# Kernel tuning notes

Hardware: AMD Instinct MI355X
Metric: run time of the kernel (lower is better)

Reference implementation:

```python
import jax, jax.numpy as jnp
import numpy as np

N_NODES = 50000
N_EDGES = 800000
NUM_GRAPHS = 128
FEAT = 128
HID = 64
NUM_LAYERS = 3
OUT = 2
K = 30
LATENT = HID * NUM_LAYERS + 1  # 193 = conv1 kernel size & stride


def _lin(k, i, o):
    s = 1.0 / np.sqrt(i)
    return jax.random.uniform(k, (i, o), jnp.float32, -s, s)


def setup_inputs() -> dict:
    key = jax.random.key(0)
    ks = jax.random.split(key, 16)
    x = jax.random.normal(ks[0], (N_NODES, FEAT), jnp.float32)
    edge_index = jax.random.randint(ks[1], (2, N_EDGES), 0, N_NODES, dtype=jnp.int64)
    batch = jnp.sort(jax.random.randint(ks[2], (N_NODES,), 0, NUM_GRAPHS, dtype=jnp.int64))
    w0 = _lin(ks[3], FEAT, HID); b0 = jnp.zeros((HID,), jnp.float32)
    w1 = _lin(ks[4], HID, HID);  b1 = jnp.zeros((HID,), jnp.float32)
    w2 = _lin(ks[5], HID, HID);  b2 = jnp.zeros((HID,), jnp.float32)
    w3 = _lin(ks[6], HID, 1);    b3 = jnp.zeros((1,), jnp.float32)
    conv1_w = jax.random.normal(ks[7], (16, 1, LATENT), jnp.float32) * (1.0 / np.sqrt(LATENT))
    conv1_b = jnp.zeros((16,), jnp.float32)
    conv2_w = jax.random.normal(ks[8], (32, 16, 5), jnp.float32) * (1.0 / np.sqrt(16 * 5))
    conv2_b = jnp.zeros((32,), jnp.float32)
    dense_dim = (int((K - 2) / 2 + 1) - 5 + 1) * 32  # 352
    lin1_w = _lin(ks[9], dense_dim, 256); lin1_b = jnp.zeros((256,), jnp.float32)
    lin2_w = _lin(ks[10], 256, OUT);      lin2_b = jnp.zeros((OUT,), jnp.float32)
    return dict(x=x, edge_index=edge_index, batch=batch,
                w0=w0, b0=b0, w1=w1, b1=b1, w2=w2, b2=b2, w3=w3, b3=b3,
                conv1_w=conv1_w, conv1_b=conv1_b, conv2_w=conv2_w, conv2_b=conv2_b,
                lin1_w=lin1_w, lin1_b=lin1_b, lin2_w=lin2_w, lin2_b=lin2_b)


def _gcn(h_in, w, b, src, dst, norm, n):
    # GCNConv: out_i = sum_j d_i^-1/2 d_j^-1/2 (x_j W) over A+I, plus bias
    h = h_in @ w
    msg = h[src] * norm[:, None]  # gather over edges (incl. self loops)
    return jax.ops.segment_sum(msg, dst, num_segments=n) + b


def _sort_pool(x, batch, k, g):
    # per-graph descending sort on last channel, top-k, zero-pad
    n, d = x.shape
    order = jnp.lexsort((-x[:, -1], batch))  # primary: batch asc, secondary: last feat desc
    xs, bs = x[order], batch[order]
    counts = jax.ops.segment_sum(jnp.ones((n,), jnp.int32), batch, num_segments=g)
    starts = jnp.cumsum(counts) - counts
    rank = jnp.arange(n) - starts[bs]
    slot = jnp.where(rank < k, rank, k)  # overflow nodes dumped in slot k (discarded)
    out = jnp.zeros((g, k + 1, d), x.dtype).at[bs, slot].set(xs)
    return out[:, :k].reshape(g, k * d)


def _conv1d(z, w, stride):
    return jax.lax.conv_general_dilated(z, w, window_strides=(stride,), padding='VALID',
                                        dimension_numbers=('NCH', 'OIH', 'NCH'))


def reference(x, edge_index, batch, w0, b0, w1, b1, w2, b2, w3, b3,
              conv1_w, conv1_b, conv2_w, conv2_b, lin1_w, lin1_b, lin2_w, lin2_b):
    n = x.shape[0]
    loop = jnp.arange(n, dtype=edge_index.dtype)
    src = jnp.concatenate([edge_index[0], loop])
    dst = jnp.concatenate([edge_index[1], loop])
    deg = jax.ops.segment_sum(jnp.ones_like(src, jnp.float32), dst, num_segments=n)
    dinv = jnp.where(deg > 0, jax.lax.rsqrt(deg), 0.0)
    norm = dinv[src] * dinv[dst]

    h1 = jnp.tanh(_gcn(x,  w0, b0, src, dst, norm, n))
    h2 = jnp.tanh(_gcn(h1, w1, b1, src, dst, norm, n))
    h3 = jnp.tanh(_gcn(h2, w2, b2, src, dst, norm, n))
    h4 = jnp.tanh(_gcn(h3, w3, b3, src, dst, norm, n))
    hcat = jnp.concatenate([h1, h2, h3, h4], axis=-1)  # [N, 193]

    p = _sort_pool(hcat, batch, K, NUM_GRAPHS)  # [G, K*193]
    z = p[:, None, :]                                   # [G, 1, K*193]
    z = jax.nn.relu(_conv1d(z, conv1_w, LATENT) + conv1_b[None, :, None])  # [G,16,K]
    g, c, l = z.shape
    z = z.reshape(g, c, l // 2, 2).max(axis=-1)         # MaxPool1d(2,2) -> [G,16,15]
    z = jax.nn.relu(_conv1d(z, conv2_w, 1) + conv2_b[None, :, None])       # [G,32,11]
    z = z.reshape(g, -1)                                # [G,352]
    z = jax.nn.relu(z @ lin1_w + lin1_b)
    # dropout is identity in eval mode
    return z @ lin2_w + lin2_b
```

## Files before the change

kernel.cpp:

```cpp
#include <hip/hip_runtime.h>
#include <math.h>

#define NGRAPH 128
#define KTOP 30
#define LATENT 193
#define HID 64

typedef unsigned short u16;

__global__ __launch_bounds__(256) void k_gemm_hist(
        const float* __restrict__ A, const float* __restrict__ W,
        float* __restrict__ Hs, int M, int K, int NG,
        const int* __restrict__ dst, const int* __restrict__ batch,
        int* edeg, u16* __restrict__ rank, int* starts,
        int E, int n, int NH) {
    __shared__ float As[64][17];
    __shared__ float Bs[16][65];
    int bid = blockIdx.x;
    if ((bid & 1) == 0) {
        int gemm_id = bid >> 1;
        if (gemm_id >= NG) return;
        int tid = threadIdx.x;
        int tx = tid & 15, ty = tid >> 4;
        int br = gemm_id * 64;
        float c[4][4] = {};
        for (int k0 = 0; k0 < K; k0 += 16) {
            {
                int idx = tid * 4;
                int r = idx >> 4;
                int kk = idx & 15;
                int grow = br + r;
                float4 v = make_float4(0.f, 0.f, 0.f, 0.f);
                if (grow < M) v = *(const float4*)(A + (size_t)grow * K + k0 + kk);
                As[r][kk + 0] = v.x; As[r][kk + 1] = v.y;
                As[r][kk + 2] = v.z; As[r][kk + 3] = v.w;
            }
            {
                int idx = tid * 4;
                int kk = idx >> 6;
                int col = idx & 63;
                float4 v = *(const float4*)(W + (size_t)(k0 + kk) * 64 + col);
                Bs[kk][col + 0] = v.x; Bs[kk][col + 1] = v.y;
                Bs[kk][col + 2] = v.z; Bs[kk][col + 3] = v.w;
            }
            __syncthreads();
#pragma unroll
            for (int kk = 0; kk < 16; ++kk) {
                float a[4], b[4];
#pragma unroll
                for (int i = 0; i < 4; i++) a[i] = As[ty + i * 16][kk];
#pragma unroll
                for (int j = 0; j < 4; j++) b[j] = Bs[kk][tx + j * 16];
#pragma unroll
                for (int i = 0; i < 4; i++)
#pragma unroll
                    for (int j = 0; j < 4; j++) c[i][j] += a[i] * b[j];
            }
            __syncthreads();
        }
#pragma unroll
        for (int i = 0; i < 4; i++) {
            int row = br + ty + i * 16;
            if (row >= M) continue;
#pragma unroll
            for (int j = 0; j < 4; j++) {
                int col = tx + j * 16;
                Hs[(size_t)row * HID + col] = c[i][j];
            }
        }
    } else {
        int fid = bid >> 1;
        if (fid >= NH) return;
        int t = threadIdx.x;
        int gi = fid * 256 + t;
        if (gi < n) {
            int b = batch[gi];
            if (gi == 0) {
                for (int g = 0; g <= b; g++) starts[g] = 0;
            } else {
                int pb = batch[gi - 1];
                for (int g = pb + 1; g <= b; g++) starts[g] = gi;
            }
            if (gi == n - 1) {
                for (int g = b + 1; g <= NGRAPH; g++) starts[g] = n;
            }
        }
        int base = fid * 1024;
#pragma unroll
        for (int k = 0; k < 4; k++) {
            int e = base + k * 256 + t;
            if (e < E) {
                int d = dst[e];
                rank[e] = (u16)atomicAdd(&edeg[d], 1);
            }
        }
    }
}

__global__ void k_scan1(const int* __restrict__ edeg, int* offs, int* bsum,
                        float* dinv, int n) {
    __shared__ int s[256];
    int t = threadIdx.x;
    int gi = blockIdx.x * 256 + t;
    int v = (gi < n) ? edeg[gi] : 0;
    if (gi < n) dinv[gi] = rsqrtf((float)(v + 1));
    s[t] = v;
    __syncthreads();
    for (int o = 1; o < 256; o <<= 1) {
        int add = (t >= o) ? s[t - o] : 0;
        __syncthreads();
        s[t] += add;
        __syncthreads();
    }
    if (gi < n) offs[gi] = s[t] - v;
    if (t == 255) bsum[blockIdx.x] = s[255];
}

__global__ void k_scan2(int* bsum, int* boff, int nb) {
    __shared__ int s[256];
    int t = threadIdx.x;
    int v = (t < nb) ? bsum[t] : 0;
    s[t] = v;
    __syncthreads();
    for (int o = 1; o < 256; o <<= 1) {
        int add = (t >= o) ? s[t - o] : 0;
        __syncthreads();
        s[t] += add;
        __syncthreads();
    }
    if (t < nb) boff[t] = s[t] - v;
}

__global__ void k_scan3(int* offs, const int* __restrict__ boff, int n, int E) {
    int gi = blockIdx.x * blockDim.x + threadIdx.x;
    if (gi < n) offs[gi] += boff[gi >> 8];
    if (gi == 0) offs[n] = E;
}

__global__ __launch_bounds__(256) void k_fill(const int* __restrict__ src,
                                              const int* __restrict__ dst,
                                              const u16* __restrict__ rank,
                                              const int* __restrict__ offs,
                                              u16* __restrict__ csr, int E) {
    int t = blockIdx.x * 256 + threadIdx.x;
    int e0 = t * 4;
    if (e0 + 4 <= E) {
        int4 s4 = *(const int4*)(src + e0);
        int4 d4 = *(const int4*)(dst + e0);
        const u16* rp = rank + e0;
        csr[offs[d4.x] + rp[0]] = (u16)s4.x;
        csr[offs[d4.y] + rp[1]] = (u16)s4.y;
        csr[offs[d4.z] + rp[2]] = (u16)s4.z;
        csr[offs[d4.w] + rp[3]] = (u16)s4.w;
    } else {
        for (int e = e0; e < E; e++)
            csr[offs[dst[e]] + rank[e]] = (u16)src[e];
    }
}

__global__ __launch_bounds__(256) void k_gemm(const float* __restrict__ A,
                                              const float* __restrict__ W,
                                              const float* __restrict__ dinv,
                                              float* __restrict__ Hs,
                                              int M, int K) {
    __shared__ float As[64][17];
    __shared__ float Bs[16][65];
    int tid = threadIdx.x;
    int tx = tid & 15, ty = tid >> 4;
    int br = blockIdx.x * 64;
    float c[4][4] = {};
    for (int k0 = 0; k0 < K; k0 += 16) {
        {
            int idx = tid * 4;
            int r = idx >> 4;
            int kk = idx & 15;
            int grow = br + r;
            float4 v = make_float4(0.f, 0.f, 0.f, 0.f);
            if (grow < M) v = *(const float4*)(A + (size_t)grow * K + k0 + kk);
            As[r][kk + 0] = v.x; As[r][kk + 1] = v.y;
            As[r][kk + 2] = v.z; As[r][kk + 3] = v.w;
        }
        {
            int idx = tid * 4;
            int kk = idx >> 6;
            int col = idx & 63;
            float4 v = *(const float4*)(W + (size_t)(k0 + kk) * 64 + col);
            Bs[kk][col + 0] = v.x; Bs[kk][col + 1] = v.y;
            Bs[kk][col + 2] = v.z; Bs[kk][col + 3] = v.w;
        }
        __syncthreads();
#pragma unroll
        for (int kk = 0; kk < 16; ++kk) {
            float a[4], b[4];
#pragma unroll
            for (int i = 0; i < 4; i++) a[i] = As[ty + i * 16][kk];
#pragma unroll
            for (int j = 0; j < 4; j++) b[j] = Bs[kk][tx + j * 16];
#pragma unroll
            for (int i = 0; i < 4; i++)
#pragma unroll
                for (int j = 0; j < 4; j++) c[i][j] += a[i] * b[j];
        }
        __syncthreads();
    }
#pragma unroll
    for (int i = 0; i < 4; i++) {
        int row = br + ty + i * 16;
        if (row >= M) continue;
        float d = dinv[row];
#pragma unroll
        for (int j = 0; j < 4; j++) {
            int col = tx + j * 16;
            Hs[(size_t)row * HID + col] = c[i][j] * d;
        }
    }
}

template <bool DEFER, bool FUSE_TS>
__global__ __launch_bounds__(256) void k_agg(const float* __restrict__ Hs,
                                             const u16* __restrict__ csr,
                                             const int* __restrict__ offs,
                                             const float* __restrict__ dinv,
                                             const float* __restrict__ b,
                                             float* __restrict__ H, int n,
                                             const float* __restrict__ w3,
                                             float* __restrict__ ts) {
    int wid = threadIdx.x >> 6;
    int lane = threadIdx.x & 63;
    int node = blockIdx.x * 4 + wid;
    if (node >= n) return;
    float d = dinv[node];
    float acc = Hs[(size_t)node * HID + lane];
    if (DEFER) acc *= d;
    int s = offs[node], e = offs[node + 1];
    int i = s;
    for (; i + 8 <= e; i += 8) {
        float part = 0.f;
#pragma unroll
        for (int k = 0; k < 8; k++) {
            int u = csr[i + k];
            float v = Hs[(size_t)u * HID + lane];
            if (DEFER) v *= dinv[u];
            part += v;
        }
        acc += part;
    }
    for (; i < e; i++) {
        int u = csr[i];
        float v = Hs[(size_t)u * HID + lane];
        if (DEFER) v *= dinv[u];
        acc += v;
    }
    float h = tanhf(acc * d + b[lane]);
    H[(size_t)node * HID + lane] = h;
    if (FUSE_TS) {
        float v = h * w3[lane];
        for (int o = 32; o > 0; o >>= 1) v += __shfl_down(v, o, 64);
        if (lane == 0) ts[node] = v * d;
    }
}

__global__ void k_agg4(const float* __restrict__ ts, const u16* __restrict__ csr,
                       const int* __restrict__ offs, const float* __restrict__ dinv,
                       const float* __restrict__ b3, float* h4, int n) {
    int node = blockIdx.x * blockDim.x + threadIdx.x;
    if (node >= n) return;
    float acc = ts[node];
    int s = offs[node], e = offs[node + 1];
    for (int i = s; i < e; i++) acc += ts[csr[i]];
    h4[node] = tanhf(acc * dinv[node] + b3[0]);
}

__global__ __launch_bounds__(512) void k_select(const float* __restrict__ h4,
                                                const int* __restrict__ starts,
                                                int* __restrict__ sel) {
    int g = blockIdx.x;
    int s = starts[g], c = starts[g + 1] - s;
    __shared__ float v[1024];
    int t = threadIdx.x;
    if (c <= 1024) {
        for (int i = t; i < c; i += 512) v[i] = h4[s + i];
        __syncthreads();
        for (int i = t; i < c; i += 512) {
            float vi = v[i];
            int r = 0;
            for (int j = 0; j < c; j++) {
                float vj = v[j];
                r += (vj > vi) || (vj == vi && j < i);
            }
            if (r < KTOP) sel[g * KTOP + r] = s + i;
        }
    } else {
        for (int i = t; i < c; i += 512) {
            float vi = h4[s + i];
            int r = 0;
            for (int j = 0; j < c; j++) {
                float vj = h4[s + j];
                r += (vj > vi) || (vj == vi && j < i);
            }
            if (r < KTOP) sel[g * KTOP + r] = s + i;
        }
    }
    for (int slot = t; slot < KTOP; slot += 512)
        if (slot >= c) sel[g * KTOP + slot] = -1;
}

__global__ __launch_bounds__(1024) void k_tail(const float* __restrict__ h1,
                                               const float* __restrict__ h2,
                                               const float* __restrict__ h3,
                                               const float* __restrict__ h4,
                                               const int* __restrict__ sel,
                                               const float* __restrict__ c1w,
                                               const float* __restrict__ c1b,
                                               const float* __restrict__ c2w,
                                               const float* __restrict__ c2b,
                                               const float* __restrict__ l1w,
                                               const float* __restrict__ l1b,
                                               const float* __restrict__ l2w,
                                               const float* __restrict__ l2b,
                                               float* __restrict__ out) {
    __shared__ float p[KTOP * LATENT];
    __shared__ float w1s[16 * LATENT];
    __shared__ float w2s[32 * 16 * 5];
    __shared__ float z1[16 * KTOP];
    __shared__ float z1p[16 * 15];
    __shared__ float flat[352];
    __shared__ float part[1024];
    __shared__ float y1[256];
    int g = blockIdx.x;
    int t = threadIdx.x;
    for (int i = t; i < 16 * LATENT; i += 1024) w1s[i] = c1w[i];
    for (int i = t; i < 32 * 16 * 5; i += 1024) w2s[i] = c2w[i];
    for (int i = t; i < KTOP * LATENT; i += 1024) {
        int slot = i / LATENT;
        int j = i - slot * LATENT;
        int node = sel[g * KTOP + slot];
        float v = 0.f;
        if (node >= 0) {
            if (j < 64)       v = h1[(size_t)node * HID + j];
            else if (j < 128) v = h2[(size_t)node * HID + j - 64];
            else if (j < 192) v = h3[(size_t)node * HID + j - 128];
            else              v = h4[node];
        }
        p[i] = v;
    }
    __syncthreads();
    if (t < 16 * KTOP) {
        int ch = t / KTOP, tt = t - ch * KTOP;
        float s = c1b[ch];
        const float* wp = &w1s[ch * LATENT];
        const float* pp = &p[tt * LATENT];
        for (int j = 0; j < LATENT; j++) s += pp[j] * wp[j];
        z1[ch * KTOP + tt] = fmaxf(s, 0.f);
    }
    __syncthreads();
    if (t < 16 * 15) {
        int ch = t / 15, tt = t - ch * 15;
        z1p[t] = fmaxf(z1[ch * KTOP + 2 * tt], z1[ch * KTOP + 2 * tt + 1]);
    }
    __syncthreads();
    if (t < 32 * 11) {
        int c2 = t / 11, tt = t - c2 * 11;
        float s = c2b[c2];
        for (int c1i = 0; c1i < 16; c1i++) {
            const float* wp = &w2s[(c2 * 16 + c1i) * 5];
            const float* zp = &z1p[c1i * 15 + tt];
#pragma unroll
            for (int dt = 0; dt < 5; dt++) s += zp[dt] * wp[dt];
        }
        flat[c2 * 11 + tt] = fmaxf(s, 0.f);
    }
    __syncthreads();
    {
        int o = t & 255, ch = t >> 8;
        int i0 = ch * 88, i1 = i0 + 88;
        float s = 0.f;
        for (int i = i0; i < i1; i++) s += flat[i] * l1w[(size_t)i * 256 + o];
        part[t] = s;
    }
    __syncthreads();
    if (t < 256)
        y1[t] = fmaxf(part[t] + part[256 + t] + part[512 + t] + part[768 + t] + l1b[t], 0.f);
    __syncthreads();
    if (t < 128) {
        int o = t >> 6, lane = t & 63;
        float s = 0.f;
        for (int i = lane; i < 256; i += 64) s += y1[i] * l2w[(size_t)i * 2 + o];
        for (int off = 32; off > 0; off >>= 1) s += __shfl_down(s, off, 64);
        if (lane == 0) out[g * 2 + o] = s + l2b[o];
    }
}

static inline char* align256(char* p) {
    return (char*)(((uintptr_t)p + 255) & ~(uintptr_t)255);
}

extern "C" void kernel_launch(void* const* d_in, const int* in_sizes, int n_in,
                              void* d_out, int out_size, void* d_ws, size_t ws_size,
                              hipStream_t stream) {
    const float* x     = (const float*)d_in[0];
    const int*  eidx   = (const int*)d_in[1];
    const int*  batch  = (const int*)d_in[2];
    const float* w0    = (const float*)d_in[3];
    const float* b0    = (const float*)d_in[4];
    const float* w1    = (const float*)d_in[5];
    const float* b1    = (const float*)d_in[6];
    const float* w2    = (const float*)d_in[7];
    const float* b2    = (const float*)d_in[8];
    const float* w3    = (const float*)d_in[9];
    const float* b3    = (const float*)d_in[10];
    const float* c1w   = (const float*)d_in[11];
    const float* c1b   = (const float*)d_in[12];
    const float* c2w   = (const float*)d_in[13];
    const float* c2b   = (const float*)d_in[14];
    const float* l1w   = (const float*)d_in[15];
    const float* l1b   = (const float*)d_in[16];
    const float* l2w   = (const float*)d_in[17];
    const float* l2b   = (const float*)d_in[18];

    int N = in_sizes[2];
    int E = in_sizes[1] / 2;
    int K0 = in_sizes[0] / N;
    const int* esrc = eidx;
    const int* edst = eidx + E;

    char* w = (char*)d_ws;
    float* dinv  = (float*)w;             w = align256(w + (size_t)N * 4);
    int*   edeg  = (int*)w;               w = align256(w + (size_t)N * 4);
    int*   offs  = (int*)w;               w = align256(w + (size_t)(N + 1) * 4);
    int*   bsum  = (int*)w;               w = align256(w + 1024);
    int*   boff  = (int*)w;               w = align256(w + 1024);
    float* ts    = (float*)w;             w = align256(w + (size_t)N * 4);
    float* h4    = (float*)w;             w = align256(w + (size_t)N * 4);
    int* starts  = (int*)w;               w = align256(w + (NGRAPH + 1) * 4);
    int* sel     = (int*)w;               w = align256(w + NGRAPH * KTOP * 4);
    u16* rank    = (u16*)w;               w = align256(w + (size_t)E * 2);
    u16* csr     = (u16*)w;               w = align256(w + (size_t)E * 2);
    float* Hs    = (float*)w;             w = align256(w + (size_t)N * HID * 4);
    float* h1    = (float*)w;             w = align256(w + (size_t)N * HID * 4);
    float* h2    = (float*)w;             w = align256(w + (size_t)N * HID * 4);
    float* h3    = (float*)w;             w = align256(w + (size_t)N * HID * 4);

    int nb = (N + 255) / 256;
    int NG = (N + 63) / 64;
    int NH = (E + 1023) / 1024;
    int agg_grid = (N + 3) / 4;

    hipMemsetAsync(edeg, 0, (size_t)N * 4, stream);

    int g1 = 2 * (NG > NH ? NG : NH);
    k_gemm_hist<<<g1, 256, 0, stream>>>(x, w0, Hs, N, K0, NG,
                                        edst, batch, edeg, rank, starts, E, N, NH);

    k_scan1<<<nb, 256, 0, stream>>>(edeg, offs, bsum, dinv, N);
    k_scan2<<<1, 256, 0, stream>>>(bsum, boff, nb);
    k_scan3<<<nb, 256, 0, stream>>>(offs, boff, N, E);

    k_fill<<<(E / 4 + 255) / 256 + 1, 256, 0, stream>>>(esrc, edst, rank, offs, csr, E);

    k_agg<true, false><<<agg_grid, 256, 0, stream>>>(Hs, csr, offs, dinv, b0, h1, N, nullptr, nullptr);
    k_gemm<<<NG, 256, 0, stream>>>(h1, w1, dinv, Hs, N, HID);
    k_agg<false, false><<<agg_grid, 256, 0, stream>>>(Hs, csr, offs, dinv, b1, h2, N, nullptr, nullptr);
    k_gemm<<<NG, 256, 0, stream>>>(h2, w2, dinv, Hs, N, HID);
    k_agg<false, true><<<agg_grid, 256, 0, stream>>>(Hs, csr, offs, dinv, b2, h3, N, w3, ts);
    k_agg4<<<(N + 255) / 256, 256, 0, stream>>>(ts, csr, offs, dinv, b3, h4, N);

    k_select<<<NGRAPH, 512, 0, stream>>>(h4, starts, sel);

    k_tail<<<NGRAPH, 1024, 0, stream>>>(h1, h2, h3, h4, sel,
                                        c1w, c1b, c2w, c2b,
                                        l1w, l1b, l2w, l2b,
                                        (float*)d_out);
}
```

Measured before the change: 262.4 us.

## Fuse select into tail, merge scan2/scan3, replace memset with kernel, interleave gemm/hist

```diff
diff --git a/kernel.cpp b/kernel.cpp
--- a/kernel.cpp
+++ b/kernel.cpp
@@ -7,19 +7,23 @@
 #define HID 64
 
 typedef unsigned short u16;
+
+__global__ void k_zero(int* edeg, int n) {
+    int i = blockIdx.x * blockDim.x + threadIdx.x;
+    if (i < n) edeg[i] = 0;
+}
 
 __global__ __launch_bounds__(256) void k_gemm_hist(
         const float* __restrict__ A, const float* __restrict__ W,
         float* __restrict__ Hs, int M, int K, int NG,
         const int* __restrict__ dst, const int* __restrict__ batch,
         int* edeg, u16* __restrict__ rank, int* starts,
-        int E, int n, int NH) {
+        int E, int n) {
     __shared__ float As[64][17];
     __shared__ float Bs[16][65];
     int bid = blockIdx.x;
-    if ((bid & 1) == 0) {
-        int gemm_id = bid >> 1;
-        if (gemm_id >= NG) return;
+    int gemm_id = (bid % 5 == 0) ? bid / 5 : -1;
+    if (gemm_id >= 0 && gemm_id < NG) {
         int tid = threadIdx.x;
         int tx = tid & 15, ty = tid >> 4;
         int br = gemm_id * 64;
@@ -69,10 +73,9 @@
             }
         }
     } else {
-        int fid = bid >> 1;
-        if (fid >= NH) return;
-        int t = threadIdx.x;
-        int gi = fid * 256 + t;
+        int ngb = min((bid + 4) / 5, NG);
+        int fid = bid - ngb;
+        int gi = fid * 256 + threadIdx.x;
         if (gi < n) {
             int b = batch[gi];
             if (gi == 0) {
@@ -85,14 +88,9 @@
                 for (int g = b + 1; g <= NGRAPH; g++) starts[g] = n;
             }
         }
-        int base = fid * 1024;
-#pragma unroll
-        for (int k = 0; k < 4; k++) {
-            int e = base + k * 256 + t;
-            if (e < E) {
-                int d = dst[e];
-                rank[e] = (u16)atomicAdd(&edeg[d], 1);
-            }
+        if (gi < E) {
+            int d = dst[gi];
+            rank[gi] = (u16)atomicAdd(&edeg[d], 1);
         }
     }
 }
@@ -116,9 +114,11 @@
     if (t == 255) bsum[blockIdx.x] = s[255];
 }
 
-__global__ void k_scan2(int* bsum, int* boff, int nb) {
+__global__ void k_scan23(int* offs, const int* __restrict__ bsum,
+                         int n, int E, int nb) {
     __shared__ int s[256];
     int t = threadIdx.x;
+    int bid = blockIdx.x;
     int v = (t < nb) ? bsum[t] : 0;
     s[t] = v;
     __syncthreads();
@@ -128,12 +128,9 @@
         s[t] += add;
         __syncthreads();
     }
-    if (t < nb) boff[t] = s[t] - v;
-}
-
-__global__ void k_scan3(int* offs, const int* __restrict__ boff, int n, int E) {
-    int gi = blockIdx.x * blockDim.x + threadIdx.x;
-    if (gi < n) offs[gi] += boff[gi >> 8];
+    int boffv = (bid == 0) ? 0 : s[bid - 1];
+    int gi = bid * 256 + t;
+    if (gi < n) offs[gi] += boffv;
     if (gi == 0) offs[n] = E;
 }
 
@@ -271,57 +268,20 @@
     h4[node] = tanhf(acc * dinv[node] + b3[0]);
 }
 
-__global__ __launch_bounds__(512) void k_select(const float* __restrict__ h4,
-                                                const int* __restrict__ starts,
-                                                int* __restrict__ sel) {
-    int g = blockIdx.x;
-    int s = starts[g], c = starts[g + 1] - s;
-    __shared__ float v[1024];
-    int t = threadIdx.x;
-    if (c <= 1024) {
-        for (int i = t; i < c; i += 512) v[i] = h4[s + i];
-        __syncthreads();
-        for (int i = t; i < c; i += 512) {
-            float vi = v[i];
-            int r = 0;
-            for (int j = 0; j < c; j++) {
-                float vj = v[j];
-                r += (vj > vi) || (vj == vi && j < i);
-            }
-            if (r < KTOP) sel[g * KTOP + r] = s + i;
-        }
-    } else {
-        for (int i = t; i < c; i += 512) {
-            float vi = h4[s + i];
-            int r = 0;
-            for (int j = 0; j < c; j++) {
-                float vj = h4[s + j];
-                r += (vj > vi) || (vj == vi && j < i);
-            }
-            if (r < KTOP) sel[g * KTOP + r] = s + i;
-        }
-    }
-    for (int slot = t; slot < KTOP; slot += 512)
-        if (slot >= c) sel[g * KTOP + slot] = -1;
-}
-
-__global__ __launch_bounds__(1024) void k_tail(const float* __restrict__ h1,
-                                               const float* __restrict__ h2,
-                                               const float* __restrict__ h3,
-                                               const float* __restrict__ h4,
-                                               const int* __restrict__ sel,
-                                               const float* __restrict__ c1w,
-                                               const float* __restrict__ c1b,
-                                               const float* __restrict__ c2w,
-                                               const float* __restrict__ c2b,
-                                               const float* __restrict__ l1w,
-                                               const float* __restrict__ l1b,
-                                               const float* __restrict__ l2w,
-                                               const float* __restrict__ l2b,
-                                               float* __restrict__ out) {
+__global__ __launch_bounds__(1024) void k_select_tail(
+        const float* __restrict__ h1, const float* __restrict__ h2,
+        const float* __restrict__ h3, const float* __restrict__ h4,
+        const int* __restrict__ starts,
+        const float* __restrict__ c1w, const float* __restrict__ c1b,
+        const float* __restrict__ c2w, const float* __restrict__ c2b,
+        const float* __restrict__ l1w, const float* __restrict__ l1b,
+        const float* __restrict__ l2w, const float* __restrict__ l2b,
+        float* __restrict__ out) {
     __shared__ float p[KTOP * LATENT];
     __shared__ float w1s[16 * LATENT];
     __shared__ float w2s[32 * 16 * 5];
+    __shared__ float vv[1024];
+    __shared__ int   sel_s[KTOP];
     __shared__ float z1[16 * KTOP];
     __shared__ float z1p[16 * 15];
     __shared__ float flat[352];
@@ -329,12 +289,42 @@
     __shared__ float y1[256];
     int g = blockIdx.x;
     int t = threadIdx.x;
+    int s = starts[g], c = starts[g + 1] - s;
+
     for (int i = t; i < 16 * LATENT; i += 1024) w1s[i] = c1w[i];
     for (int i = t; i < 32 * 16 * 5; i += 1024) w2s[i] = c2w[i];
+    if (t < KTOP) sel_s[t] = -1;
+
+    if (c <= 1024) {
+        for (int i = t; i < c; i += 1024) vv[i] = h4[s + i];
+        __syncthreads();
+        for (int i = t; i < c; i += 1024) {
+            float vi = vv[i];
+            int r = 0;
+            for (int j = 0; j < c; j++) {
+                float vj = vv[j];
+                r += (vj > vi) || (vj == vi && j < i);
+            }
+            if (r < KTOP) sel_s[r] = s + i;
+        }
+    } else {
+        __syncthreads();
+        for (int i = t; i < c; i += 1024) {
+            float vi = h4[s + i];
+            int r = 0;
+            for (int j = 0; j < c; j++) {
+                float vj = h4[s + j];
+                r += (vj > vi) || (vj == vi && j < i);
+            }
+            if (r < KTOP) sel_s[r] = s + i;
+        }
+    }
+    __syncthreads();
+
     for (int i = t; i < KTOP * LATENT; i += 1024) {
         int slot = i / LATENT;
         int j = i - slot * LATENT;
-        int node = sel[g * KTOP + slot];
+        int node = sel_s[slot];
         float v = 0.f;
         if (node >= 0) {
             if (j < 64)       v = h1[(size_t)node * HID + j];
@@ -347,11 +337,11 @@
     __syncthreads();
     if (t < 16 * KTOP) {
         int ch = t / KTOP, tt = t - ch * KTOP;
-        float s = c1b[ch];
+        float sa = c1b[ch];
         const float* wp = &w1s[ch * LATENT];
         const float* pp = &p[tt * LATENT];
-        for (int j = 0; j < LATENT; j++) s += pp[j] * wp[j];
-        z1[ch * KTOP + tt] = fmaxf(s, 0.f);
+        for (int j = 0; j < LATENT; j++) sa += pp[j] * wp[j];
+        z1[ch * KTOP + tt] = fmaxf(sa, 0.f);
     }
     __syncthreads();
     if (t < 16 * 15) {
@@ -361,22 +351,22 @@
     __syncthreads();
     if (t < 32 * 11) {
         int c2 = t / 11, tt = t - c2 * 11;
-        float s = c2b[c2];
+        float sa = c2b[c2];
         for (int c1i = 0; c1i < 16; c1i++) {
             const float* wp = &w2s[(c2 * 16 + c1i) * 5];
             const float* zp = &z1p[c1i * 15 + tt];
 #pragma unroll
-            for (int dt = 0; dt < 5; dt++) s += zp[dt] * wp[dt];
-        }
-        flat[c2 * 11 + tt] = fmaxf(s, 0.f);
+            for (int dt = 0; dt < 5; dt++) sa += zp[dt] * wp[dt];
+        }
+        flat[c2 * 11 + tt] = fmaxf(sa, 0.f);
     }
     __syncthreads();
     {
         int o = t & 255, ch = t >> 8;
         int i0 = ch * 88, i1 = i0 + 88;
-        float s = 0.f;
-        for (int i = i0; i < i1; i++) s += flat[i] * l1w[(size_t)i * 256 + o];
-        part[t] = s;
+        float sa = 0.f;
+        for (int i = i0; i < i1; i++) sa += flat[i] * l1w[(size_t)i * 256 + o];
+        part[t] = sa;
     }
     __syncthreads();
     if (t < 256)
@@ -384,10 +374,10 @@
     __syncthreads();
     if (t < 128) {
         int o = t >> 6, lane = t & 63;
-        float s = 0.f;
-        for (int i = lane; i < 256; i += 64) s += y1[i] * l2w[(size_t)i * 2 + o];
-        for (int off = 32; off > 0; off >>= 1) s += __shfl_down(s, off, 64);
-        if (lane == 0) out[g * 2 + o] = s + l2b[o];
+        float sa = 0.f;
+        for (int i = lane; i < 256; i += 64) sa += y1[i] * l2w[(size_t)i * 2 + o];
+        for (int off = 32; off > 0; off >>= 1) sa += __shfl_down(sa, off, 64);
+        if (lane == 0) out[g * 2 + o] = sa + l2b[o];
     }
 }
 
@@ -429,11 +419,9 @@
     int*   edeg  = (int*)w;               w = align256(w + (size_t)N * 4);
     int*   offs  = (int*)w;               w = align256(w + (size_t)(N + 1) * 4);
     int*   bsum  = (int*)w;               w = align256(w + 1024);
-    int*   boff  = (int*)w;               w = align256(w + 1024);
     float* ts    = (float*)w;             w = align256(w + (size_t)N * 4);
     float* h4    = (float*)w;             w = align256(w + (size_t)N * 4);
     int* starts  = (int*)w;               w = align256(w + (NGRAPH + 1) * 4);
-    int* sel     = (int*)w;               w = align256(w + NGRAPH * KTOP * 4);
     u16* rank    = (u16*)w;               w = align256(w + (size_t)E * 2);
     u16* csr     = (u16*)w;               w = align256(w + (size_t)E * 2);
     float* Hs    = (float*)w;             w = align256(w + (size_t)N * HID * 4);
@@ -443,18 +431,16 @@
 
     int nb = (N + 255) / 256;
     int NG = (N + 63) / 64;
-    int NH = (E + 1023) / 1024;
+    int NH = (E + 255) / 256;
     int agg_grid = (N + 3) / 4;
 
-    hipMemsetAsync(edeg, 0, (size_t)N * 4, stream);
-
-    int g1 = 2 * (NG > NH ? NG : NH);
-    k_gemm_hist<<<g1, 256, 0, stream>>>(x, w0, Hs, N, K0, NG,
-                                        edst, batch, edeg, rank, starts, E, N, NH);
+    k_zero<<<nb, 256, 0, stream>>>(edeg, N);
+
+    k_gemm_hist<<<NG + NH, 256, 0, stream>>>(x, w0, Hs, N, K0, NG,
+                                             edst, batch, edeg, rank, starts, E, N);
 
     k_scan1<<<nb, 256, 0, stream>>>(edeg, offs, bsum, dinv, N);
-    k_scan2<<<1, 256, 0, stream>>>(bsum, boff, nb);
-    k_scan3<<<nb, 256, 0, stream>>>(offs, boff, N, E);
+    k_scan23<<<nb, 256, 0, stream>>>(offs, bsum, N, E, nb);
 
     k_fill<<<(E / 4 + 255) / 256 + 1, 256, 0, stream>>>(esrc, edst, rank, offs, csr, E);
 
@@ -463,12 +449,10 @@
     k_agg<false, false><<<agg_grid, 256, 0, stream>>>(Hs, csr, offs, dinv, b1, h2, N, nullptr, nullptr);
     k_gemm<<<NG, 256, 0, stream>>>(h2, w2, dinv, Hs, N, HID);
     k_agg<false, true><<<agg_grid, 256, 0, stream>>>(Hs, csr, offs, dinv, b2, h3, N, w3, ts);
-    k_agg4<<<(N + 255) / 256, 256, 0, stream>>>(ts, csr, offs, dinv, b3, h4, N);
-
-    k_select<<<NGRAPH, 512, 0, stream>>>(h4, starts, sel);
-
-    k_tail<<<NGRAPH, 1024, 0, stream>>>(h1, h2, h3, h4, sel,
-                                        c1w, c1b, c2w, c2b,
-                                        l1w, l1b, l2w, l2b,
-                                        (float*)d_out);
-}
+    k_agg4<<<nb, 256, 0, stream>>>(ts, csr, offs, dinv, b3, h4, N);
+
+    k_select_tail<<<NGRAPH, 1024, 0, stream>>>(h1, h2, h3, h4, starts,
+                                               c1w, c1b, c2w, c2b,
+                                               l1w, l1b, l2w, l2b,
+                                               (float*)d_out);
+}
```

Measured after the change: 273.3 us. 4.2% more time.
